# Kernel optimization log

Measured on AMD Instinct MI355X. Metric: run time of the kernel, lower is better.

The kernel has to match this reference:

```python
import jax, jax.numpy as jnp
import numpy as np

EPS = 1e-6

def _rmsnorm(x, w):
    var = jnp.mean(x * x, axis=-1, keepdims=True)
    return x * jax.lax.rsqrt(var + EPS) * w

def setup_inputs() -> dict:
    key = jax.random.key(0)
    ks = jax.random.split(key, 10)
    B, S, D = 2, 2048, 1024
    H, E, F = 16, 8, 4096
    std = 0.02
    return {
        "x": jax.random.normal(ks[0], (B, S, D), dtype=jnp.float32),
        "ln1_w": jnp.ones((D,), dtype=jnp.float32),
        "ln2_w": jnp.ones((D,), dtype=jnp.float32),
        "wq": jax.random.normal(ks[1], (D, D), dtype=jnp.float32) * std,
        "wk": jax.random.normal(ks[2], (D, D), dtype=jnp.float32) * std,
        "wv": jax.random.normal(ks[3], (D, D), dtype=jnp.float32) * std,
        "wo": jax.random.normal(ks[4], (D, D), dtype=jnp.float32) * std,
        "wr": jax.random.normal(ks[5], (D, E), dtype=jnp.float32) * std,
        "w1": jax.random.normal(ks[6], (E, D, F), dtype=jnp.float32) * std,
        "w2": jax.random.normal(ks[7], (E, F, D), dtype=jnp.float32) * std,
    }

def reference(x, ln1_w, ln2_w, wq, wk, wv, wo, wr, w1, w2):
    B, S, D = x.shape
    H = 16
    Dh = D // H
    E = wr.shape[1]
    K = 2
    Z_COEF = 0.001

    # --- bidirectional attention sublayer ---
    residual = x
    xn = _rmsnorm(x, ln1_w)
    q = (xn @ wq).reshape(B, S, H, Dh).transpose(0, 2, 1, 3)  # [B,H,S,Dh]
    k = (xn @ wk).reshape(B, S, H, Dh).transpose(0, 2, 1, 3)
    v = (xn @ wv).reshape(B, S, H, Dh).transpose(0, 2, 1, 3)
    scale = 1.0 / jnp.sqrt(jnp.asarray(Dh, dtype=x.dtype))
    scores = jnp.einsum("bhqd,bhkd->bhqk", q, k) * scale  # non-causal
    attn = jax.nn.softmax(scores, axis=-1)
    ctx = jnp.einsum("bhqk,bhkd->bhqd", attn, v)
    attn_out = ctx.transpose(0, 2, 1, 3).reshape(B, S, D) @ wo
    x = residual + attn_out

    # --- MoE sublayer ---
    residual = x
    xn2 = _rmsnorm(x, ln2_w)
    logits = xn2 @ wr                       # [B,S,E]
    probs = jax.nn.softmax(logits, axis=-1)
    topv, topi = jax.lax.top_k(probs, K)    # [B,S,K]
    weights = topv / jnp.sum(topv, axis=-1, keepdims=True)
    onehot = jax.nn.one_hot(topi, E, dtype=x.dtype)          # [B,S,K,E]
    dispatch = jnp.sum(onehot * weights[..., None], axis=-2)  # [B,S,E] combine weights

    # router losses: switch-style load balance + z-loss
    frac_tokens = jnp.mean(jnp.sum(onehot, axis=-2), axis=(0, 1))  # [E]
    frac_probs = jnp.mean(probs, axis=(0, 1))                      # [E]
    aux_loss = E * jnp.sum(frac_tokens * frac_probs) / K
    z = jax.nn.logsumexp(logits, axis=-1)
    router_loss = aux_loss + Z_COEF * jnp.mean(z * z)

    # expert-grouped FFN: dense per expert, masked combine (loop over fixed E)
    expert_out = jnp.zeros_like(xn2)
    for e in range(E):
        h = jax.nn.gelu(xn2 @ w1[e])
        expert_out = expert_out + dispatch[..., e:e + 1] * (h @ w2[e])

    out = residual + expert_out
    return out, router_loss
```

## Files before the change

### kernel.cpp

```cpp
#include <hip/hip_runtime.h>
#include <hip/hip_bf16.h>
#include <math.h>
#include <stdint.h>

#define DEV static __device__ __forceinline__

typedef __attribute__((ext_vector_type(8))) short short8;
typedef __attribute__((ext_vector_type(8))) unsigned short ushort8;
typedef __attribute__((ext_vector_type(4))) float floatx4;

using bf16 = __hip_bfloat16;

constexpr int Bc = 2, Sc = 2048, Dc = 1024, Hc = 16, DHc = 64, Ec = 8, Fc = 4096;
constexpr int Tc = Bc * Sc;

DEV floatx4 mfma_bf16(short8 a, short8 b, floatx4 c) {
  return __builtin_amdgcn_mfma_f32_16x16x32_bf16(a, b, c, 0, 0, 0);
}

DEV float gelu_tanh(float x) {
  float z = 0.7978845608028654f * (x + 0.044715f * x * x * x);
  z = fminf(fmaxf(z, -15.f), 15.f);
  float t = __expf(2.f * z);
  return 0.5f * x * (1.f + (t - 1.f) / (t + 1.f));
}

DEV void gl16(const void* g, void* l) {
  __builtin_amdgcn_global_load_lds(
      reinterpret_cast<const __attribute__((address_space(1))) void*>(
          reinterpret_cast<uintptr_t>(g)),
      reinterpret_cast<__attribute__((address_space(3))) void*>(
          reinterpret_cast<uintptr_t>(l)),
      16, 0, 0);
}

DEV void tr_tile(const float* __restrict__ W, bf16* __restrict__ Wt,
                 int K, int N, bf16 (*Ts)[72]) {
  const int n0 = blockIdx.x * 64, k0 = blockIdx.y * 64;
  const int tid = threadIdx.x;
#pragma unroll
  for (int it = 0; it < 4; it++) {
    int u = tid + it * 256;
    int r = u >> 4, c4 = (u & 15) << 2;
    floatx4 v = *(const floatx4*)(W + (size_t)(k0 + r) * N + n0 + c4);
#pragma unroll
    for (int j = 0; j < 4; j++) Ts[c4 + j][r] = __float2bfloat16(v[j]);
  }
  __syncthreads();
#pragma unroll
  for (int it = 0; it < 2; it++) {
    int u = tid + it * 256;
    int rn = u >> 3, kc = (u & 7) << 3;
    *(short8*)(Wt + (size_t)(n0 + rn) * K + k0 + kc) = *(const short8*)(&Ts[rn][kc]);
  }
}

__global__ __launch_bounds__(256) void k_wt(const float* __restrict__ W,
                                            bf16* __restrict__ Wt, int K, int N) {
  __shared__ __align__(16) bf16 Ts[64][72];
  const size_t mb = (size_t)blockIdx.z * K * N;
  tr_tile(W + mb, Wt + mb, K, N, Ts);
}

__global__ __launch_bounds__(256) void k_wt4(
    const float* __restrict__ a, const float* __restrict__ b,
    const float* __restrict__ c, const float* __restrict__ d,
    bf16* __restrict__ o) {
  __shared__ __align__(16) bf16 Ts[64][72];
  const int z = blockIdx.z;
  const float* W = z == 0 ? a : (z == 1 ? b : (z == 2 ? c : d));
  tr_tile(W, o + (size_t)z * Dc * Dc, Dc, Dc, Ts);
}

DEV void gemm_core(bf16* As, bf16* Bs,
                   const bf16* __restrict__ A, int lda, int m0,
                   const bf16* __restrict__ Bt, int ldb, int n0,
                   int Kdim, floatx4 (&acc)[4][4]) {
  const int tid = threadIdx.x;
  const int lane = tid & 63;
  const int wave = tid >> 6;
  const int wm = wave & 1, wn = wave >> 1;
  const int l15 = lane & 15, quad = lane >> 4;

#pragma unroll
  for (int mi = 0; mi < 4; mi++)
#pragma unroll
    for (int ni = 0; ni < 4; ni++)
#pragma unroll
      for (int r = 0; r < 4; r++) acc[mi][ni][r] = 0.f;

  const int arow = tid >> 3;
  const int akc = (tid & 7) << 3;
  const int nK = Kdim >> 6;
  for (int kb = 0; kb < nK; kb++) {
    const int k0 = kb << 6;
    __syncthreads();
#pragma unroll
    for (int it = 0; it < 4; it++) {
      const int row = arow + it * 32;
      const int lbase = (it * 256 + wave * 64) * 8;
      gl16(A + (size_t)(m0 + row) * lda + k0 + akc, As + lbase);
      gl16(Bt + (size_t)(n0 + row) * ldb + k0 + akc, Bs + lbase);
    }
    __syncthreads();
#pragma unroll
    for (int kk = 0; kk < 64; kk += 32) {
      short8 af[4], bfr[4];
#pragma unroll
      for (int mi = 0; mi < 4; mi++)
        af[mi] = *(const short8*)(As + (wm * 64 + mi * 16 + l15) * 64 + kk + quad * 8);
#pragma unroll
      for (int ni = 0; ni < 4; ni++)
        bfr[ni] = *(const short8*)(Bs + (wn * 64 + ni * 16 + l15) * 64 + kk + quad * 8);
#pragma unroll
      for (int mi = 0; mi < 4; mi++)
#pragma unroll
        for (int ni = 0; ni < 4; ni++)
          acc[mi][ni] = mfma_bf16(af[mi], bfr[ni], acc[mi][ni]);
    }
  }
}

#define GEMM_SHARED \
  __shared__ __align__(16) bf16 As[128 * 64]; \
  __shared__ __align__(16) bf16 Bs[128 * 64];
#define LANE_DECODE \
  const int tid = threadIdx.x; const int lane = tid & 63; const int wave = tid >> 6; \
  const int wm = wave & 1, wn = wave >> 1; const int l15 = lane & 15, quad = lane >> 4; \
  (void)tid; (void)lane;

__global__ __launch_bounds__(256) void k_rms(const float* __restrict__ x,
                                             const float* __restrict__ w,
                                             bf16* __restrict__ out,
                                             float* __restrict__ outf) {
  __shared__ float red[4];
  const int tid = threadIdx.x, lane = tid & 63, wave = tid >> 6;
  const size_t base = (size_t)blockIdx.x * Dc + tid * 4;
  floatx4 v = *(const floatx4*)(x + base);
  float ss = v[0] * v[0] + v[1] * v[1] + v[2] * v[2] + v[3] * v[3];
#pragma unroll
  for (int off = 32; off >= 1; off >>= 1) ss += __shfl_xor(ss, off);
  if (lane == 0) red[wave] = ss;
  __syncthreads();
  float tot = red[0] + red[1] + red[2] + red[3];
  float rr = rsqrtf(tot * (1.f / Dc) + 1e-6f);
  floatx4 wv = *(const floatx4*)(w + tid * 4);
  floatx4 res;
#pragma unroll
  for (int j = 0; j < 4; j++) res[j] = v[j] * rr * wv[j];
#pragma unroll
  for (int j = 0; j < 4; j++) out[base + j] = __float2bfloat16(res[j]);
  if (outf) *(floatx4*)(outf + base) = res;
}

__global__ __launch_bounds__(256) void k_gemm_qkv(
    const bf16* __restrict__ xn, const bf16* __restrict__ wt,
    bf16* __restrict__ q, bf16* __restrict__ k, bf16* __restrict__ v) {
  GEMM_SHARED; LANE_DECODE;
  const bf16* W = wt + (size_t)blockIdx.z * Dc * Dc;
  bf16* out = blockIdx.z == 0 ? q : (blockIdx.z == 1 ? k : v);
  const int m0 = blockIdx.y * 128, n0 = blockIdx.x * 128;
  floatx4 acc[4][4];
  gemm_core(As, Bs, xn, Dc, m0, W, Dc, n0, Dc, acc);
#pragma unroll
  for (int mi = 0; mi < 4; mi++)
#pragma unroll
    for (int ni = 0; ni < 4; ni++)
#pragma unroll
      for (int r = 0; r < 4; r++) {
        int row = m0 + wm * 64 + mi * 16 + quad * 4 + r;
        int col = n0 + wn * 64 + ni * 16 + l15;
        int b = row >> 11, s = row & 2047, h = col >> 6, dh = col & 63;
        out[((((size_t)b * Hc + h) * Sc + s) << 6) + dh] = __float2bfloat16(acc[mi][ni][r]);
      }
}

__global__ __launch_bounds__(256) void k_gemm_wo(
    const bf16* __restrict__ ctx, const bf16* __restrict__ wot,
    const float* __restrict__ x, float* __restrict__ x1) {
  GEMM_SHARED; LANE_DECODE;
  const int m0 = blockIdx.y * 128, n0 = blockIdx.x * 128;
  floatx4 acc[4][4];
  gemm_core(As, Bs, ctx, Dc, m0, wot, Dc, n0, Dc, acc);
#pragma unroll
  for (int mi = 0; mi < 4; mi++)
#pragma unroll
    for (int ni = 0; ni < 4; ni++)
#pragma unroll
      for (int r = 0; r < 4; r++) {
        int row = m0 + wm * 64 + mi * 16 + quad * 4 + r;
        int col = n0 + wn * 64 + ni * 16 + l15;
        size_t idx = (size_t)row * Dc + col;
        x1[idx] = acc[mi][ni][r] + x[idx];
      }
}

__global__ __launch_bounds__(256) void k_attn(
    const bf16* __restrict__ Q, const bf16* __restrict__ K,
    const bf16* __restrict__ V, bf16* __restrict__ ctx) {
  __shared__ __align__(16) bf16 Ks[32 * 72];
  __shared__ __align__(16) bf16 Vs[64 * 40];
  __shared__ __align__(16) bf16 Ps[4 * 16 * 40];
  const int tid = threadIdx.x, lane = tid & 63, wave = tid >> 6;
  const int l15 = lane & 15, quad = lane >> 4;
  const int bh = blockIdx.y;
  const size_t base = (size_t)bh * Sc * DHc;
  const bf16* Qb = Q + base; const bf16* Kb = K + base; const bf16* Vb = V + base;
  const int q0 = blockIdx.x * 64 + wave * 16;
  bf16* Pw = Ps + wave * (16 * 40);

  short8 aq[2];
#pragma unroll
  for (int kk2 = 0; kk2 < 2; kk2++)
    aq[kk2] = *(const short8*)(Qb + (size_t)(q0 + l15) * 64 + kk2 * 32 + quad * 8);

  float m_i[4], l_i[4];
  floatx4 o[4];
#pragma unroll
  for (int r = 0; r < 4; r++) { m_i[r] = -__builtin_inff(); l_i[r] = 0.f; }
#pragma unroll
  for (int n4 = 0; n4 < 4; n4++)
#pragma unroll
    for (int r = 0; r < 4; r++) o[n4][r] = 0.f;

  for (int kt = 0; kt < Sc / 32; kt++) {
    const int kb = kt * 32;
    __syncthreads();
    {
      int row = tid >> 3, kc = (tid & 7) << 3;
      *(short8*)(Ks + row * 72 + kc) = *(const short8*)(Kb + (size_t)(kb + row) * 64 + kc);
    }
    if (tid < 128) {
      int kp = tid >> 3, dg = tid & 7;
      ushort8 a0 = *(const ushort8*)(Vb + (size_t)(kb + 2 * kp) * 64 + dg * 8);
      ushort8 a1 = *(const ushort8*)(Vb + (size_t)(kb + 2 * kp + 1) * 64 + dg * 8);
#pragma unroll
      for (int j = 0; j < 8; j++) {
        int dh = dg * 8 + j;
        int elem = dh * 40 + ((((kp >> 2) ^ (dh >> 3)) & 3) << 3) + ((kp & 3) << 1);
        *(unsigned int*)(Vs + elem) = (unsigned int)a0[j] | ((unsigned int)a1[j] << 16);
      }
    }
    __syncthreads();
    floatx4 sc[2];
#pragma unroll
    for (int ni = 0; ni < 2; ni++) {
#pragma unroll
      for (int r = 0; r < 4; r++) sc[ni][r] = 0.f;
#pragma unroll
      for (int kk2 = 0; kk2 < 2; kk2++) {
        short8 bk = *(const short8*)(Ks + (ni * 16 + l15) * 72 + kk2 * 32 + quad * 8);
        sc[ni] = mfma_bf16(aq[kk2], bk, sc[ni]);
      }
    }
#pragma unroll
    for (int ni = 0; ni < 2; ni++)
#pragma unroll
      for (int r = 0; r < 4; r++) sc[ni][r] *= 0.125f;
    float rmax[4];
#pragma unroll
    for (int r = 0; r < 4; r++) rmax[r] = fmaxf(sc[0][r], sc[1][r]);
#pragma unroll
    for (int off = 1; off < 16; off <<= 1)
#pragma unroll
      for (int r = 0; r < 4; r++) rmax[r] = fmaxf(rmax[r], __shfl_xor(rmax[r], off));
    float alpha[4], rsum[4];
#pragma unroll
    for (int r = 0; r < 4; r++) {
      float nm = fmaxf(m_i[r], rmax[r]);
      alpha[r] = __expf(m_i[r] - nm);
      m_i[r] = nm;
    }
#pragma unroll
    for (int ni = 0; ni < 2; ni++)
#pragma unroll
      for (int r = 0; r < 4; r++) sc[ni][r] = __expf(sc[ni][r] - m_i[r]);
#pragma unroll
    for (int r = 0; r < 4; r++) rsum[r] = sc[0][r] + sc[1][r];
#pragma unroll
    for (int off = 1; off < 16; off <<= 1)
#pragma unroll
      for (int r = 0; r < 4; r++) rsum[r] += __shfl_xor(rsum[r], off);
#pragma unroll
    for (int r = 0; r < 4; r++) l_i[r] = l_i[r] * alpha[r] + rsum[r];
#pragma unroll
    for (int n4 = 0; n4 < 4; n4++)
#pragma unroll
      for (int r = 0; r < 4; r++) o[n4][r] *= alpha[r];
#pragma unroll
    for (int ni = 0; ni < 2; ni++)
#pragma unroll
      for (int r = 0; r < 4; r++)
        Pw[(quad * 4 + r) * 40 + ni * 16 + l15] = __float2bfloat16(sc[ni][r]);
    __syncthreads();
    short8 ap = *(const short8*)(Pw + l15 * 40 + quad * 8);
#pragma unroll
    for (int n4 = 0; n4 < 4; n4++) {
      int dh = n4 * 16 + l15;
      short8 bv = *(const short8*)(Vs + dh * 40 + (((quad ^ (dh >> 3)) & 3) << 3));
      o[n4] = mfma_bf16(ap, bv, o[n4]);
    }
  }
  const int b = bh >> 4, h = bh & 15;
#pragma unroll
  for (int n4 = 0; n4 < 4; n4++)
#pragma unroll
    for (int r = 0; r < 4; r++) {
      int s = q0 + quad * 4 + r;
      int d = h * 64 + n4 * 16 + l15;
      ctx[(size_t)(b * Sc + s) * Dc + d] = __float2bfloat16(o[n4][r] / l_i[r]);
    }
}

__global__ __launch_bounds__(256) void k_router(
    const float* __restrict__ xn2f, const float* __restrict__ wr,
    int* __restrict__ topi, float* __restrict__ topw,
    int* __restrict__ counts, float* __restrict__ sum_probs,
    float* __restrict__ sum_z2) {
  __shared__ float sp[8]; __shared__ float sz[1]; __shared__ int scnt[8];
  const int tid = threadIdx.x, wave = tid >> 6, lane = tid & 63;
  if (tid < 8) { sp[tid] = 0.f; scnt[tid] = 0; }
  if (tid == 0) sz[0] = 0.f;
  __syncthreads();
  const int t = blockIdx.x * 4 + wave;
  float a[8];
#pragma unroll
  for (int e = 0; e < 8; e++) a[e] = 0.f;
  const float* xr = xn2f + (size_t)t * Dc;
#pragma unroll 4
  for (int i = 0; i < 16; i++) {
    int d = lane + i * 64;
    float xv = xr[d];
    floatx4 wa = *(const floatx4*)(wr + d * 8);
    floatx4 wb = *(const floatx4*)(wr + d * 8 + 4);
#pragma unroll
    for (int e = 0; e < 4; e++) a[e] += xv * wa[e];
#pragma unroll
    for (int e = 0; e < 4; e++) a[e + 4] += xv * wb[e];
  }
#pragma unroll
  for (int off = 1; off < 64; off <<= 1)
#pragma unroll
    for (int e = 0; e < 8; e++) a[e] += __shfl_xor(a[e], off);
  float mx = a[0];
#pragma unroll
  for (int e = 1; e < 8; e++) mx = fmaxf(mx, a[e]);
  float pr[8], sum = 0.f;
#pragma unroll
  for (int e = 0; e < 8; e++) { pr[e] = __expf(a[e] - mx); sum += pr[e]; }
  float inv = 1.f / sum;
#pragma unroll
  for (int e = 0; e < 8; e++) pr[e] *= inv;
  float lse = mx + logf(sum);
  int i0 = 0; float p0 = pr[0];
#pragma unroll
  for (int e = 1; e < 8; e++) if (pr[e] > p0) { p0 = pr[e]; i0 = e; }
  int i1 = -1; float p1 = -1.f;
#pragma unroll
  for (int e = 0; e < 8; e++) if (e != i0 && pr[e] > p1) { p1 = pr[e]; i1 = e; }
  float wsum = p0 + p1;
  if (lane == 0) {
    topi[2 * t] = i0; topi[2 * t + 1] = i1;
    topw[2 * t] = p0 / wsum; topw[2 * t + 1] = p1 / wsum;
    atomicAdd(&scnt[i0], 1); atomicAdd(&scnt[i1], 1);
#pragma unroll
    for (int e = 0; e < 8; e++) atomicAdd(&sp[e], pr[e]);
    atomicAdd(&sz[0], lse * lse);
  }
  __syncthreads();
  if (tid < 8) { atomicAdd(&counts[tid], scnt[tid]); atomicAdd(&sum_probs[tid], sp[tid]); }
  if (tid == 0) atomicAdd(sum_z2, sz[0]);
}

__global__ void k_meta(const int* __restrict__ counts, int* __restrict__ offs,
                       const float* __restrict__ sum_probs,
                       const float* __restrict__ sum_z2, float* __restrict__ loss_out) {
  float aux = 0.f;
  offs[0] = 0;
  for (int e = 0; e < 8; e++) {
    offs[e + 1] = offs[e] + counts[e];
    aux += ((float)counts[e] / Tc) * (sum_probs[e] / Tc);
  }
  float loss = (float)Ec * aux * 0.5f + 0.001f * (sum_z2[0] / Tc);
  loss_out[0] = loss;
}

__global__ __launch_bounds__(256) void k_gather(
    const bf16* __restrict__ xn2, const int* __restrict__ topi,
    const int* __restrict__ offs, int* __restrict__ cursors,
    int* __restrict__ rowpos, bf16* __restrict__ Ag) {
  const int tid = threadIdx.x, wave = tid >> 6, lane = tid & 63;
  const int t = blockIdx.x * 4 + wave;
  const int i0 = topi[2 * t], i1 = topi[2 * t + 1];
  int r0 = 0, r1 = 0;
  if (lane == 0) {
    r0 = atomicAdd(&cursors[i0], 1);
    r1 = atomicAdd(&cursors[i1], 1);
    rowpos[2 * t] = r0; rowpos[2 * t + 1] = r1;
  }
  r0 = __shfl(r0, 0); r1 = __shfl(r1, 0);
  const short8* src = (const short8*)(xn2 + (size_t)t * Dc);
  short8 c0 = src[lane], c1 = src[lane + 64];
  short8* d0 = (short8*)(Ag + (size_t)(offs[i0] + r0) * Dc);
  short8* d1 = (short8*)(Ag + (size_t)(offs[i1] + r1) * Dc);
  d0[lane] = c0; d0[lane + 64] = c1;
  d1[lane] = c0; d1[lane + 64] = c1;
}

__global__ __launch_bounds__(256) void k_ffn1(
    const bf16* __restrict__ Ag, const bf16* __restrict__ w1t,
    bf16* __restrict__ Hb, const int* __restrict__ offs) {
  const int e = blockIdx.z;
  const int cnt = offs[e + 1] - offs[e];
  const int m0 = blockIdx.y * 128;
  if (m0 >= cnt) return;
  GEMM_SHARED; LANE_DECODE;
  const int n0 = blockIdx.x * 128;
  const bf16* A = Ag + (size_t)offs[e] * Dc;
  const bf16* W = w1t + (size_t)e * Dc * Fc;
  bf16* Hp = Hb + (size_t)offs[e] * Fc;
  floatx4 acc[4][4];
  gemm_core(As, Bs, A, Dc, m0, W, Dc, n0, Dc, acc);
#pragma unroll
  for (int mi = 0; mi < 4; mi++)
#pragma unroll
    for (int ni = 0; ni < 4; ni++)
#pragma unroll
      for (int r = 0; r < 4; r++) {
        int row = m0 + wm * 64 + mi * 16 + quad * 4 + r;
        int col = n0 + wn * 64 + ni * 16 + l15;
        if (row < cnt)
          Hp[(size_t)row * Fc + col] = __float2bfloat16(gelu_tanh(acc[mi][ni][r]));
      }
}

__global__ __launch_bounds__(256) void k_ffn2(
    const bf16* __restrict__ Hb, const bf16* __restrict__ w2t,
    float* __restrict__ Ob, const int* __restrict__ offs) {
  const int e = blockIdx.z;
  const int cnt = offs[e + 1] - offs[e];
  const int m0 = blockIdx.y * 128;
  if (m0 >= cnt) return;
  GEMM_SHARED; LANE_DECODE;
  const int n0 = blockIdx.x * 128;
  const bf16* A = Hb + (size_t)offs[e] * Fc;
  const bf16* W = w2t + (size_t)e * Fc * Dc;
  float* Op = Ob + (size_t)offs[e] * Dc;
  floatx4 acc[4][4];
  gemm_core(As, Bs, A, Fc, m0, W, Fc, n0, Fc, acc);
#pragma unroll
  for (int mi = 0; mi < 4; mi++)
#pragma unroll
    for (int ni = 0; ni < 4; ni++)
#pragma unroll
      for (int r = 0; r < 4; r++) {
        int row = m0 + wm * 64 + mi * 16 + quad * 4 + r;
        int col = n0 + wn * 64 + ni * 16 + l15;
        if (row < cnt) Op[(size_t)row * Dc + col] = acc[mi][ni][r];
      }
}

__global__ __launch_bounds__(256) void k_combine(
    const float* __restrict__ x1, const float* __restrict__ Ob,
    const int* __restrict__ topi, const float* __restrict__ topw,
    const int* __restrict__ rowpos, const int* __restrict__ offs,
    float* __restrict__ out) {
  const int t = blockIdx.x, tid = threadIdx.x;
  const int i0 = topi[2 * t], i1 = topi[2 * t + 1];
  const float w0 = topw[2 * t], w1 = topw[2 * t + 1];
  const float* o0 = Ob + (size_t)(offs[i0] + rowpos[2 * t]) * Dc;
  const float* o1 = Ob + (size_t)(offs[i1] + rowpos[2 * t + 1]) * Dc;
  const float* xr = x1 + (size_t)t * Dc;
  floatx4 a = *(const floatx4*)(xr + tid * 4);
  floatx4 b = *(const floatx4*)(o0 + tid * 4);
  floatx4 c = *(const floatx4*)(o1 + tid * 4);
  floatx4 res;
#pragma unroll
  for (int j = 0; j < 4; j++) res[j] = a[j] + w0 * b[j] + w1 * c[j];
  *(floatx4*)(out + (size_t)t * Dc + tid * 4) = res;
}

extern "C" void kernel_launch(void* const* d_in, const int* in_sizes, int n_in,
                              void* d_out, int out_size, void* d_ws, size_t ws_size,
                              hipStream_t stream) {
  (void)in_sizes; (void)n_in; (void)out_size; (void)ws_size;
  const float* x    = (const float*)d_in[0];
  const float* ln1w = (const float*)d_in[1];
  const float* ln2w = (const float*)d_in[2];
  const float* wq   = (const float*)d_in[3];
  const float* wk   = (const float*)d_in[4];
  const float* wv   = (const float*)d_in[5];
  const float* wo   = (const float*)d_in[6];
  const float* wr   = (const float*)d_in[7];
  const float* w1   = (const float*)d_in[8];
  const float* w2   = (const float*)d_in[9];
  float* out = (float*)d_out;

  char* p = (char*)d_ws;
  auto take = [&](size_t bytes) {
    char* r = p; p += (bytes + 255) & ~(size_t)255; return r;
  };
  bf16*  xn   = (bf16*)take((size_t)Tc * Dc * 2);
  bf16*  qb   = (bf16*)take((size_t)Tc * Dc * 2);
  bf16*  kb   = (bf16*)take((size_t)Tc * Dc * 2);
  bf16*  vb   = (bf16*)take((size_t)Tc * Dc * 2);
  bf16*  ctx  = (bf16*)take((size_t)Tc * Dc * 2);
  float* x1   = (float*)take((size_t)Tc * Dc * 4);
  bf16*  xn2  = (bf16*)take((size_t)Tc * Dc * 2);
  float* xn2f = (float*)take((size_t)Tc * Dc * 4);
  bf16*  Ag   = (bf16*)take((size_t)2 * Tc * Dc * 2);
  bf16*  Hb   = (bf16*)take((size_t)2 * Tc * Fc * 2);
  float* Ob   = (float*)take((size_t)2 * Tc * Dc * 4);
  bf16*  wtqkvo = (bf16*)take((size_t)4 * Dc * Dc * 2);
  bf16*  wtbig  = (bf16*)take((size_t)Ec * (size_t)Dc * Fc * 2);
  int*   counts    = (int*)take(512);
  int*   cursors   = counts + 8;
  float* sum_probs = (float*)(counts + 16);
  float* sum_z2    = sum_probs + 8;
  int*   offs      = (int*)take(256);
  int*   topi      = (int*)take((size_t)2 * Tc * 4);
  float* topw      = (float*)take((size_t)2 * Tc * 4);
  int*   rowpos    = (int*)take((size_t)2 * Tc * 4);

  hipMemsetAsync(counts, 0, 512, stream);

  k_wt4<<<dim3(Dc / 64, Dc / 64, 4), 256, 0, stream>>>(wq, wk, wv, wo, wtqkvo);
  k_wt<<<dim3(Fc / 64, Dc / 64, Ec), 256, 0, stream>>>(w1, wtbig, Dc, Fc);

  k_rms<<<Tc, 256, 0, stream>>>(x, ln1w, xn, nullptr);
  k_gemm_qkv<<<dim3(Dc / 128, Tc / 128, 3), 256, 0, stream>>>(xn, wtqkvo, qb, kb, vb);
  k_attn<<<dim3(Sc / 64, Bc * Hc), 256, 0, stream>>>(qb, kb, vb, ctx);
  k_gemm_wo<<<dim3(Dc / 128, Tc / 128), 256, 0, stream>>>(ctx, wtqkvo + (size_t)3 * Dc * Dc, x, x1);
  k_rms<<<Tc, 256, 0, stream>>>(x1, ln2w, xn2, xn2f);
  k_router<<<Tc / 4, 256, 0, stream>>>(xn2f, wr, topi, topw, counts, sum_probs, sum_z2);
  k_meta<<<1, 1, 0, stream>>>(counts, offs, sum_probs, sum_z2, out + (size_t)Tc * Dc);
  k_gather<<<Tc / 4, 256, 0, stream>>>(xn2, topi, offs, cursors, rowpos, Ag);
  k_ffn1<<<dim3(Fc / 128, Tc / 128, Ec), 256, 0, stream>>>(Ag, wtbig, Hb, offs);
  k_wt<<<dim3(Dc / 64, Fc / 64, Ec), 256, 0, stream>>>(w2, wtbig, Fc, Dc);
  k_ffn2<<<dim3(Dc / 128, Tc / 128, Ec), 256, 0, stream>>>(Hb, wtbig, Ob, offs);
  k_combine<<<Tc, 256, 0, stream>>>(x1, Ob, topi, topw, rowpos, offs, out);
}
```

Measured before the change: 1.082 ms.

## Double-buffer GEMM LDS tiles with XOR swizzle and XCD-aware block remap

The shared GEMM core now keeps two LDS buffers and issues the global-to-LDS loads for the next K tile before computing the current one. This drops one barrier per iteration and overlaps memory with MFMA work. The LDS layout is XOR-swizzled by row to cut bank conflicts on fragment reads. A block-index remap spreads contiguous tiles across the 8 XCDs for better L2 locality. In exchange, LDS use per block doubles, which may lower occupancy.

```diff
diff --git a/kernel.cpp b/kernel.cpp
--- a/kernel.cpp
+++ b/kernel.cpp
@@ -92,42 +92,59 @@
   const int arow = tid >> 3;
   const int akc = (tid & 7) << 3;
   const int nK = Kdim >> 6;
-  for (int kb = 0; kb < nK; kb++) {
+
+  auto stage = [&](int buf, int kb) {
     const int k0 = kb << 6;
-    __syncthreads();
+    const int lb0 = buf * (128 * 64);
 #pragma unroll
     for (int it = 0; it < 4; it++) {
       const int row = arow + it * 32;
-      const int lbase = (it * 256 + wave * 64) * 8;
-      gl16(A + (size_t)(m0 + row) * lda + k0 + akc, As + lbase);
-      gl16(Bt + (size_t)(n0 + row) * ldb + k0 + akc, Bs + lbase);
-    }
-    __syncthreads();
+      const int sk = k0 + (akc ^ ((row & 7) << 3));
+      const int lbase = lb0 + (it * 256 + wave * 64) * 8;
+      gl16(A + (size_t)(m0 + row) * lda + sk, As + lbase);
+      gl16(Bt + (size_t)(n0 + row) * ldb + sk, Bs + lbase);
+    }
+  };
+
+  stage(0, 0);
+  __syncthreads();
+  for (int kb = 0; kb < nK; kb++) {
+    const int cur = kb & 1;
+    if (kb + 1 < nK) stage(cur ^ 1, kb + 1);
+    const int lb0 = cur * (128 * 64);
 #pragma unroll
     for (int kk = 0; kk < 64; kk += 32) {
+      const int swk = (kk + quad * 8) ^ ((l15 & 7) << 3);
       short8 af[4], bfr[4];
 #pragma unroll
       for (int mi = 0; mi < 4; mi++)
-        af[mi] = *(const short8*)(As + (wm * 64 + mi * 16 + l15) * 64 + kk + quad * 8);
+        af[mi] = *(const short8*)(As + lb0 + (wm * 64 + mi * 16 + l15) * 64 + swk);
 #pragma unroll
       for (int ni = 0; ni < 4; ni++)
-        bfr[ni] = *(const short8*)(Bs + (wn * 64 + ni * 16 + l15) * 64 + kk + quad * 8);
+        bfr[ni] = *(const short8*)(Bs + lb0 + (wn * 64 + ni * 16 + l15) * 64 + swk);
 #pragma unroll
       for (int mi = 0; mi < 4; mi++)
 #pragma unroll
         for (int ni = 0; ni < 4; ni++)
           acc[mi][ni] = mfma_bf16(af[mi], bfr[ni], acc[mi][ni]);
     }
+    __syncthreads();
   }
 }
 
 #define GEMM_SHARED \
-  __shared__ __align__(16) bf16 As[128 * 64]; \
-  __shared__ __align__(16) bf16 Bs[128 * 64];
+  __shared__ __align__(16) bf16 As[2 * 128 * 64]; \
+  __shared__ __align__(16) bf16 Bs[2 * 128 * 64];
 #define LANE_DECODE \
   const int tid = threadIdx.x; const int lane = tid & 63; const int wave = tid >> 6; \
   const int wm = wave & 1, wn = wave >> 1; const int l15 = lane & 15, quad = lane >> 4; \
   (void)tid; (void)lane;
+#define XCD_SWZ(GX, GY) \
+  int bx, by; { \
+    constexpr int nwg = (GX) * (GY); \
+    int flat = blockIdx.y * (GX) + blockIdx.x; \
+    int wg = (flat & 7) * (nwg >> 3) + (flat >> 3); \
+    bx = wg % (GX); by = wg / (GX); }
 
 __global__ __launch_bounds__(256) void k_rms(const float* __restrict__ x,
                                              const float* __restrict__ w,
@@ -157,9 +174,10 @@
     const bf16* __restrict__ xn, const bf16* __restrict__ wt,
     bf16* __restrict__ q, bf16* __restrict__ k, bf16* __restrict__ v) {
   GEMM_SHARED; LANE_DECODE;
+  XCD_SWZ(Dc / 128, Tc / 128);
   const bf16* W = wt + (size_t)blockIdx.z * Dc * Dc;
   bf16* out = blockIdx.z == 0 ? q : (blockIdx.z == 1 ? k : v);
-  const int m0 = blockIdx.y * 128, n0 = blockIdx.x * 128;
+  const int m0 = by * 128, n0 = bx * 128;
   floatx4 acc[4][4];
   gemm_core(As, Bs, xn, Dc, m0, W, Dc, n0, Dc, acc);
 #pragma unroll
@@ -179,7 +197,8 @@
     const bf16* __restrict__ ctx, const bf16* __restrict__ wot,
     const float* __restrict__ x, float* __restrict__ x1) {
   GEMM_SHARED; LANE_DECODE;
-  const int m0 = blockIdx.y * 128, n0 = blockIdx.x * 128;
+  XCD_SWZ(Dc / 128, Tc / 128);
+  const int m0 = by * 128, n0 = bx * 128;
   floatx4 acc[4][4];
   gemm_core(As, Bs, ctx, Dc, m0, wot, Dc, n0, Dc, acc);
 #pragma unroll
@@ -412,10 +431,11 @@
     bf16* __restrict__ Hb, const int* __restrict__ offs) {
   const int e = blockIdx.z;
   const int cnt = offs[e + 1] - offs[e];
-  const int m0 = blockIdx.y * 128;
+  XCD_SWZ(Fc / 128, Tc / 128);
+  const int m0 = by * 128;
   if (m0 >= cnt) return;
   GEMM_SHARED; LANE_DECODE;
-  const int n0 = blockIdx.x * 128;
+  const int n0 = bx * 128;
   const bf16* A = Ag + (size_t)offs[e] * Dc;
   const bf16* W = w1t + (size_t)e * Dc * Fc;
   bf16* Hp = Hb + (size_t)offs[e] * Fc;
@@ -439,10 +459,11 @@
     float* __restrict__ Ob, const int* __restrict__ offs) {
   const int e = blockIdx.z;
   const int cnt = offs[e + 1] - offs[e];
-  const int m0 = blockIdx.y * 128;
+  XCD_SWZ(Dc / 128, Tc / 128);
+  const int m0 = by * 128;
   if (m0 >= cnt) return;
   GEMM_SHARED; LANE_DECODE;
-  const int n0 = blockIdx.x * 128;
+  const int n0 = bx * 128;
   const bf16* A = Hb + (size_t)offs[e] * Fc;
   const bf16* W = w2t + (size_t)e * Fc * Dc;
   float* Op = Ob + (size_t)offs[e] * Dc;
```

Measured after the change: 1.376 ms. 1.27x slower.
